# Optimization experiments

Hardware: AMD Instinct MI355X
Metric: run time of the kernel (lower is better)

## Reference

```python
import jax, jax.numpy as jnp
import numpy as np

B, L, V = 128, 32, 10000
IC, WD, H = 2048, 512, 512  # image_code_dim, word_dim, hidden_size (num_layers=1)
D = WD + IC  # GRU input dim


def setup_inputs() -> dict:
    key = jax.random.key(0)
    ks = jax.random.split(key, 10)
    image_code = jax.random.normal(ks[0], (B, IC), dtype=jnp.float32)
    captions = jax.random.randint(ks[1], (B, L), 0, V)
    cap_lens = jax.random.randint(ks[2], (B,), 2, L + 1)
    cap_lens = cap_lens.at[0].set(L)  # pin max length -> static T = L-1
    # parameters (embed/fc match init_weights uniform(-0.1,0.1); GRU/init_state ~ small random)
    embed_w = jax.random.uniform(ks[3], (V, WD), minval=-0.1, maxval=0.1, dtype=jnp.float32)
    W_ih = jax.random.normal(ks[4], (3 * H, D), dtype=jnp.float32) * 0.02
    W_hh = jax.random.normal(ks[5], (3 * H, H), dtype=jnp.float32) * 0.02
    b_ih = jnp.zeros((3 * H,), dtype=jnp.float32)
    b_hh = jnp.zeros((3 * H,), dtype=jnp.float32)
    fc_w = jax.random.uniform(ks[6], (V, H), minval=-0.1, maxval=0.1, dtype=jnp.float32)
    fc_b = jnp.zeros((V,), dtype=jnp.float32)
    init_w = jax.random.normal(ks[7], (H, IC), dtype=jnp.float32) * 0.02  # num_layers*H x IC
    init_b = jnp.zeros((H,), dtype=jnp.float32)
    return {"image_code": image_code, "captions": captions, "cap_lens": cap_lens,
            "embed_w": embed_w, "W_ih": W_ih, "W_hh": W_hh, "b_ih": b_ih, "b_hh": b_hh,
            "fc_w": fc_w, "fc_b": fc_b, "init_w": init_w, "init_b": init_b}


def _gru_decode(image_code, captions_s, lengths, h0, embed_w, W_ih, W_hh, b_ih, b_hh, fc_w, fc_b):
    T = L - 1
    emb = embed_w[captions_s]                      # (B, L, WD)
    xs = jnp.concatenate([
        jnp.broadcast_to(image_code[None], (T, B, IC)),
        jnp.transpose(emb[:, :T, :], (1, 0, 2)),   # (T, B, WD)
    ], axis=-1)                                    # (T, B, D)

    def step(h, x_t):
        gi = x_t @ W_ih.T + b_ih                   # (B, 3H)
        gh = h @ W_hh.T + b_hh                     # (B, 3H)
        i_r, i_z, i_n = jnp.split(gi, 3, axis=-1)
        h_r, h_z, h_n = jnp.split(gh, 3, axis=-1)
        r = jax.nn.sigmoid(i_r + h_r)
        z = jax.nn.sigmoid(i_z + h_z)
        n = jnp.tanh(i_n + r * h_n)
        h_new = (1.0 - z) * n + z * h
        return h_new, h_new

    _, outs = jax.lax.scan(step, h0, xs)           # (T, B, H)
    preds = jnp.einsum('tbh,vh->tbv', outs, fc_w) + fc_b  # dropout is identity in eval
    mask = jnp.arange(T)[:, None] < lengths[None, :]      # (T, B): only active steps
    preds = jnp.where(mask[:, :, None], preds, 0.0)
    return jnp.transpose(preds, (1, 0, 2))         # (B, T, V)


def reference(image_code, captions, cap_lens, embed_w, W_ih, W_hh, b_ih, b_hh, fc_w, fc_b, init_w, init_b):
    order = jnp.argsort(-cap_lens)                 # descending sort like torch.sort(..., True)
    sorted_lens = cap_lens[order]
    captions_s = captions[order]
    image_code_s = image_code[order]
    h0 = image_code_s @ init_w.T + init_b          # (B, H) (num_layers = 1)
    lengths = sorted_lens - 1
    predictions = _gru_decode(image_code_s, captions_s, lengths, h0,
                              embed_w, W_ih, W_hh, b_ih, b_hh, fc_w, fc_b)
    return predictions, captions_s, lengths, order
```

## Files before the change

### kernel.cpp

```cpp
#include <hip/hip_runtime.h>
#include <math.h>

#define B_   128
#define L_   32
#define T_   31
#define V_   10000
#define IC_  2048
#define WD_  512
#define H_   512
#define D_   2560
#define G3_  1536
#define NPAD_ 10112
#define NPROD_ 64
#define NCONS_ 158
#define NTEAM_ 2
#define SU_PFX0 1
#define SU_FCW0 17
#define SU_WHH0 (SU_FCW0 + 2528)
#define SU_N    (SU_WHH0 + 384)

typedef short short8 __attribute__((ext_vector_type(8)));
typedef float f32x4  __attribute__((ext_vector_type(4)));
typedef unsigned short ushort_t;
typedef unsigned long long ull_t;

__device__ __forceinline__ unsigned short f2bf(float f) {
    unsigned int u = __builtin_bit_cast(unsigned int, f);
    unsigned int r = (u + 0x7FFFu + ((u >> 16) & 1u)) >> 16;
    return (unsigned short)r;
}
__device__ __forceinline__ float bf2f(unsigned short h) {
    unsigned int u = ((unsigned int)h) << 16;
    return __builtin_bit_cast(float, u);
}
__device__ __forceinline__ f32x4 mfma16(short8 a, short8 b, f32x4 c) {
    return __builtin_amdgcn_mfma_f32_16x16x32_bf16(a, b, c, 0, 0, 0);
}

#define WS_ORDER  0
#define WS_LEN    512
#define WS_TOK    1024
#define WS_BAR    16896
#define WS_GIIMG  16960
#define WS_WHH    803392
#define WS_GIFULL 2376256
#define WS_OUTS   14565952
#define WS_FCW    18760256

template<bool F32>
__device__ __forceinline__ uint4 load_cvt(const void* src, size_t off) {
    if constexpr (!F32) {
        return *(const uint4*)((const unsigned short*)src + off);
    } else {
        const float* p = (const float*)src + off;
        const float4 x = *(const float4*)p;
        const float4 y = *(const float4*)(p + 4);
        union { unsigned short u[8]; uint4 v; } r;
        r.u[0]=f2bf(x.x); r.u[1]=f2bf(x.y); r.u[2]=f2bf(x.z); r.u[3]=f2bf(x.w);
        r.u[4]=f2bf(y.x); r.u[5]=f2bf(y.y); r.u[6]=f2bf(y.z); r.u[7]=f2bf(y.w);
        return r.v;
    }
}

__global__ __launch_bounds__(256) void k_setup(
    const int* __restrict__ captions,
    const int* __restrict__ cap_lens,
    const float* __restrict__ fc_w,
    const float* __restrict__ W_hh,
    const float* __restrict__ image_code,
    const float* __restrict__ W_ih,
    const float* __restrict__ b_ih,
    const float* __restrict__ init_w,
    const float* __restrict__ init_b,
    ushort_t* __restrict__ fcw_bf,
    ushort_t* __restrict__ whh_bf,
    float* __restrict__ gi_img,
    ushort_t* __restrict__ outs,
    int* __restrict__ order,
    int* __restrict__ len_i,
    int* __restrict__ tok,
    int* __restrict__ bar,
    float* __restrict__ out_tail)
{
    __shared__ __align__(16) ushort_t As[128 * 32];
    __shared__ __align__(16) ushort_t Bs[128 * 32];
    __shared__ int s_len[B_];
    __shared__ int s_ord[B_];
    const int bid = blockIdx.x;
    const int tid = threadIdx.x;

    if (bid >= SU_FCW0 && bid < SU_WHH0) {
        const int idx = (bid - SU_FCW0) * 256 + tid;
        const int row = idx >> 6;
        const int ch  = idx & 63;
        union { unsigned short u[8]; uint4 v; } r;
        if (row < V_) {
            const float* p = fc_w + (size_t)row * 512 + ch * 8;
            const float4 x = *(const float4*)p;
            const float4 y = *(const float4*)(p + 4);
            r.u[0]=f2bf(x.x); r.u[1]=f2bf(x.y); r.u[2]=f2bf(x.z); r.u[3]=f2bf(x.w);
            r.u[4]=f2bf(y.x); r.u[5]=f2bf(y.y); r.u[6]=f2bf(y.z); r.u[7]=f2bf(y.w);
        } else {
            r.v = make_uint4(0, 0, 0, 0);
        }
        *(uint4*)&fcw_bf[(size_t)row * 512 + ch * 8] = r.v;
        return;
    }
    if (bid >= SU_WHH0) {
        const int idx = (bid - SU_WHH0) * 256 + tid;
        const size_t o = (size_t)idx * 8;
        const int g = (int)(o / (48 * 512));
        const int rem = (int)(o % (48 * 512));
        const int j = rem >> 9;
        const int k = rem & 511;
        const int srow = (j >> 4) * 512 + g * 16 + (j & 15);
        const float* p = W_hh + (size_t)srow * 512 + k;
        const float4 x = *(const float4*)p;
        const float4 y = *(const float4*)(p + 4);
        union { unsigned short u[8]; uint4 v; } r;
        r.u[0]=f2bf(x.x); r.u[1]=f2bf(x.y); r.u[2]=f2bf(x.z); r.u[3]=f2bf(x.w);
        r.u[4]=f2bf(y.x); r.u[5]=f2bf(y.y); r.u[6]=f2bf(y.z); r.u[7]=f2bf(y.w);
        *(uint4*)&whh_bf[o] = r.v;
        return;
    }

    if (tid < B_) s_len[tid] = cap_lens[tid];
    __syncthreads();
    if (tid < B_) {
        const int myl = s_len[tid];
        int rank = 0;
        for (int k = 0; k < B_; ++k) {
            const int lk = s_len[k];
            if (lk > myl || (lk == myl && k < tid)) rank++;
        }
        s_ord[rank] = tid;
    }
    __syncthreads();

    if (bid == 0) {
        if (tid == 0) *bar = 0;
        if (tid < B_) {
            const int o = s_ord[tid];
            order[tid] = o;
            const int ln = s_len[o] - 1;
            len_i[tid] = ln;
            out_tail[B_ * L_ + tid]      = (float)ln;
            out_tail[B_ * L_ + B_ + tid] = (float)o;
        }
        __syncthreads();
        for (int i = tid; i < B_ * L_; i += 256) {
            const int b = i / L_, l = i % L_;
            const int c = captions[s_ord[b] * L_ + l];
            out_tail[i] = (float)c;
            if (l < T_) tok[l * B_ + b] = c;
        }
        return;
    }

    const int px = bid - SU_PFX0;
    const bool isH0 = px >= 12;
    const float* Bm = isH0 ? init_w : W_ih;
    const int ldb = isH0 ? IC_ : D_;
    const int n0 = isH0 ? (px - 12) * 128 : px * 128;
    const float* bias = isH0 ? init_b : b_ih;

    const int w = tid >> 6, lane = tid & 63, quad = lane >> 4, lr = lane & 15;
    const int srow = tid >> 2, ch = tid & 3;
    const int wm = (w & 1) * 64, wn = (w >> 1) * 64;

    const int ar0 = s_ord[srow];
    const int ar1 = s_ord[srow + 64];
    const int br0 = n0 + srow, br1 = n0 + srow + 64;

    f32x4 acc[4][4];
    const f32x4 z4 = {0.f, 0.f, 0.f, 0.f};
#pragma unroll
    for (int i = 0; i < 4; ++i)
#pragma unroll
        for (int j = 0; j < 4; ++j) acc[i][j] = z4;

    uint4 a0 = load_cvt<true>(image_code, (size_t)ar0 * IC_ + ch * 8);
    uint4 a1 = load_cvt<true>(image_code, (size_t)ar1 * IC_ + ch * 8);
    uint4 b0 = load_cvt<true>(Bm, (size_t)br0 * ldb + ch * 8);
    uint4 b1 = load_cvt<true>(Bm, (size_t)br1 * ldb + ch * 8);

    for (int k0 = 0; k0 < IC_; k0 += 32) {
        __syncthreads();
        *(uint4*)&As[(srow)      * 32 + ch * 8] = a0;
        *(uint4*)&As[(srow + 64) * 32 + ch * 8] = a1;
        *(uint4*)&Bs[(srow)      * 32 + ch * 8] = b0;
        *(uint4*)&Bs[(srow + 64) * 32 + ch * 8] = b1;
        __syncthreads();
        short8 af[4], bfr[4];
#pragma unroll
        for (int i = 0; i < 4; ++i) af[i]  = *(const short8*)&As[(wm + i * 16 + lr) * 32 + quad * 8];
#pragma unroll
        for (int j = 0; j < 4; ++j) bfr[j] = *(const short8*)&Bs[(wn + j * 16 + lr) * 32 + quad * 8];
        if (k0 + 32 < IC_) {
            a0 = load_cvt<true>(image_code, (size_t)ar0 * IC_ + k0 + 32 + ch * 8);
            a1 = load_cvt<true>(image_code, (size_t)ar1 * IC_ + k0 + 32 + ch * 8);
            b0 = load_cvt<true>(Bm, (size_t)br0 * ldb + k0 + 32 + ch * 8);
            b1 = load_cvt<true>(Bm, (size_t)br1 * ldb + k0 + 32 + ch * 8);
        }
#pragma unroll
        for (int i = 0; i < 4; ++i)
#pragma unroll
            for (int j = 0; j < 4; ++j) acc[i][j] = mfma16(af[i], bfr[j], acc[i][j]);
    }

#pragma unroll
    for (int i = 0; i < 4; ++i)
#pragma unroll
        for (int r = 0; r < 4; ++r) {
            const int m = wm + i * 16 + quad * 4 + r;
#pragma unroll
            for (int j = 0; j < 4; ++j) {
                const int n = n0 + wn + j * 16 + lr;
                const float v = acc[i][j][r] + bias[n];
                if (isH0) outs[(size_t)m * H_ + n] = f2bf(v);
                else      gi_img[(size_t)m * G3_ + n] = v;
            }
        }
}

struct EpiAdd2D {
    ushort_t* C; int ldc; const float* add; int addld; const float* bhh;
    __device__ void operator()(int m, int n, float v) const {
        const float extra = (n < 1024) ? bhh[n] : 0.f;
        C[(size_t)m * ldc + n] = f2bf(v + add[(size_t)(m & 127) * addld + n] + extra);
    }
};

template<bool AF32, bool BF32, class Epi>
__global__ __launch_bounds__(256) void gemm128(
    const void* __restrict__ A, int lda, const int* __restrict__ gidx,
    const void* __restrict__ Bm, int ldb, int K, Epi epi)
{
    __shared__ ushort_t As[128 * 32];
    __shared__ ushort_t Bs[128 * 32];
    const int tid = threadIdx.x;
    const int m0 = blockIdx.y * 128, n0 = blockIdx.x * 128;
    const int w = tid >> 6, lane = tid & 63, quad = lane >> 4, lr = lane & 15;
    const int srow = tid >> 2, ch = tid & 3;
    const int wm = (w & 1) * 64, wn = (w >> 1) * 64;

    const int ar0 = gidx ? gidx[m0 + srow]      : (m0 + srow);
    const int ar1 = gidx ? gidx[m0 + srow + 64] : (m0 + srow + 64);
    const int br0 = n0 + srow, br1 = n0 + srow + 64;

    f32x4 acc[4][4];
    const f32x4 z4 = {0.f, 0.f, 0.f, 0.f};
#pragma unroll
    for (int i = 0; i < 4; ++i)
#pragma unroll
        for (int j = 0; j < 4; ++j) acc[i][j] = z4;

    uint4 a0 = load_cvt<AF32>(A, (size_t)ar0 * lda + ch * 8);
    uint4 a1 = load_cvt<AF32>(A, (size_t)ar1 * lda + ch * 8);
    uint4 b0 = load_cvt<BF32>(Bm, (size_t)br0 * ldb + ch * 8);
    uint4 b1 = load_cvt<BF32>(Bm, (size_t)br1 * ldb + ch * 8);

    for (int k0 = 0; k0 < K; k0 += 32) {
        __syncthreads();
        *(uint4*)&As[(srow)      * 32 + ch * 8] = a0;
        *(uint4*)&As[(srow + 64) * 32 + ch * 8] = a1;
        *(uint4*)&Bs[(srow)      * 32 + ch * 8] = b0;
        *(uint4*)&Bs[(srow + 64) * 32 + ch * 8] = b1;
        __syncthreads();
        short8 af[4], bfr[4];
#pragma unroll
        for (int i = 0; i < 4; ++i) af[i]  = *(const short8*)&As[(wm + i * 16 + lr) * 32 + quad * 8];
#pragma unroll
        for (int j = 0; j < 4; ++j) bfr[j] = *(const short8*)&Bs[(wn + j * 16 + lr) * 32 + quad * 8];
        if (k0 + 32 < K) {
            a0 = load_cvt<AF32>(A, (size_t)ar0 * lda + k0 + 32 + ch * 8);
            a1 = load_cvt<AF32>(A, (size_t)ar1 * lda + k0 + 32 + ch * 8);
            b0 = load_cvt<BF32>(Bm, (size_t)br0 * ldb + k0 + 32 + ch * 8);
            b1 = load_cvt<BF32>(Bm, (size_t)br1 * ldb + k0 + 32 + ch * 8);
        }
#pragma unroll
        for (int i = 0; i < 4; ++i)
#pragma unroll
            for (int j = 0; j < 4; ++j) acc[i][j] = mfma16(af[i], bfr[j], acc[i][j]);
    }

#pragma unroll
    for (int i = 0; i < 4; ++i)
#pragma unroll
        for (int r = 0; r < 4; ++r) {
            const int m = m0 + wm + i * 16 + quad * 4 + r;
#pragma unroll
            for (int j = 0; j < 4; ++j) {
                const int n = n0 + wn + j * 16 + lr;
                epi(m, n, acc[i][j][r]);
            }
        }
}

#define PBS_STR 520
__global__ __launch_bounds__(256, 1) void k_fused(
    const ushort_t* __restrict__ whh_bf,
    const ushort_t* __restrict__ gi_full,
    const float* __restrict__ b_hh,
    ushort_t* __restrict__ outs,
    const ushort_t* __restrict__ fcw_bf,
    const float* __restrict__ fc_b,
    const int* __restrict__ len_i,
    float* __restrict__ out,
    int* __restrict__ sync)
{
    __shared__ __align__(16) ushort_t sm[43008];
    const int bid = blockIdx.x;
    const int tid = threadIdx.x;
    const int w = tid >> 6, lane = tid & 63, quad = lane >> 4, lr = lane & 15;

    if (bid < NPROD_) {
        __builtin_amdgcn_s_setprio(1);
        const int g = bid & 31;
        const int ih = bid >> 5;
        const bool leader = (bid == (ih << 5));
        ushort_t* Bs = sm;

        const ushort_t* wsrc = whh_bf + (size_t)g * 48 * 512;
        for (int i = tid; i < 48 * 64; i += 256) {
            const int row = i >> 6, c = i & 63;
            *(uint4*)&Bs[row * PBS_STR + c * 8] = *(const uint4*)&wsrc[row * 512 + c * 8];
        }
        const int cg = g * 16 + lr;
        const float bhn = b_hh[1024 + cg];
        __syncthreads();

        float hold_reg[4];
        {
            const ushort_t* h0p = outs + (size_t)ih * 64 * 512;
#pragma unroll
            for (int r = 0; r < 4; ++r)
                hold_reg[r] = bf2f(h0p[(size_t)(w * 16 + quad * 4 + r) * 512 + cg]);
        }
        ushort_t gi0[4], gi1[4], gi2[4];
#pragma unroll
        for (int r = 0; r < 4; ++r) {
            const int b = ih * 64 + w * 16 + quad * 4 + r;
            const ushort_t* p = gi_full + (size_t)b * G3_ + cg;
            gi0[r] = p[0]; gi1[r] = p[512]; gi2[r] = p[1024];
        }

        for (int step = 0; step < T_; ++step) {
            const ushort_t* hsrc = outs + (size_t)step * (128 * 512) + (size_t)ih * 64 * 512;

            uint4 hv[16];
            const ushort_t* hrow = hsrc + (size_t)(w * 16 + lr) * 512 + quad * 8;
#pragma unroll
            for (int kk = 0; kk < 16; ++kk)
                hv[kk] = *(const uint4*)(hrow + kk * 32);

            f32x4 acc[3];
#pragma unroll
            for (int j = 0; j < 3; ++j) acc[j] = (f32x4){0.f, 0.f, 0.f, 0.f};
#pragma unroll
            for (int kk = 0; kk < 16; ++kk) {
                union { uint4 v; short8 s; } cc; cc.v = hv[kk];
                const short8 af = cc.s;
#pragma unroll
                for (int j = 0; j < 3; ++j) {
                    const short8 bf = *(const short8*)&Bs[(j * 16 + lr) * PBS_STR + kk * 32 + quad * 8];
                    acc[j] = mfma16(af, bf, acc[j]);
                }
            }

            ushort_t* hdst = outs + (size_t)(step + 1) * (128 * 512);
#pragma unroll
            for (int r = 0; r < 4; ++r) {
                const int b = ih * 64 + w * 16 + quad * 4 + r;
                const float ir  = bf2f(gi0[r]);
                const float iz  = bf2f(gi1[r]);
                const float in_ = bf2f(gi2[r]);
                const float hr = acc[0][r];
                const float hz = acc[1][r];
                const float hn = acc[2][r] + bhn;
                const float rg = 1.f / (1.f + __expf(-(ir + hr)));
                const float zg = 1.f / (1.f + __expf(-(iz + hz)));
                const float nn = tanhf(in_ + rg * hn);
                const float hnew = (1.f - zg) * nn + zg * hold_reg[r];
                const unsigned int hb = (unsigned int)f2bf(hnew);
                hold_reg[r] = bf2f((unsigned short)hb);
                const unsigned int pv = (unsigned int)__shfl_xor((int)hb, 1);
                if ((lr & 1) == 0) {
                    const unsigned int word = hb | (pv << 16);
                    __hip_atomic_store((unsigned int*)&hdst[(size_t)b * 512 + cg], word,
                                       __ATOMIC_RELAXED, __HIP_MEMORY_SCOPE_AGENT);
                }
            }

            asm volatile("s_waitcnt vmcnt(0)" ::: "memory");
            __syncthreads();
            const int tgt = step + 1;
            if (tid == 0)
                __hip_atomic_store(&sync[bid * 8], tgt,
                                   __ATOMIC_RELAXED, __HIP_MEMORY_SCOPE_AGENT);

            ushort_t ng0[4], ng1[4], ng2[4];
            if (step + 1 < T_) {
                const size_t gb = (size_t)(step + 1) * 128 * G3_;
#pragma unroll
                for (int r = 0; r < 4; ++r) {
                    const int b = ih * 64 + w * 16 + quad * 4 + r;
                    const ushort_t* p = gi_full + gb + (size_t)b * G3_ + cg;
                    ng0[r] = p[0]; ng1[r] = p[512]; ng2[r] = p[1024];
                }
            }
            asm volatile("" ::: "memory");

            if (w == 0 && (step < T_ - 1 || leader)) {
                const int* pf = &sync[(ih * 32 + (lane & 31)) * 8];
                for (;;) {
                    const int v = __hip_atomic_load(pf, __ATOMIC_RELAXED, __HIP_MEMORY_SCOPE_AGENT);
                    if (__all(v >= tgt)) break;
                    __builtin_amdgcn_s_sleep(1);
                }
                if (leader && lane == 0) {
#pragma unroll
                    for (int k = 0; k < 8; ++k)
                        __hip_atomic_store(&sync[768 + k * 16 + ih], tgt,
                                           __ATOMIC_RELAXED, __HIP_MEMORY_SCOPE_AGENT);
                }
            }
            __syncthreads();
            asm volatile("" ::: "memory");

            if (step + 1 < T_) {
#pragma unroll
                for (int r = 0; r < 4; ++r) { gi0[r] = ng0[r]; gi1[r] = ng1[r]; gi2[r] = ng2[r]; }
            }
        }
    } else {
        const int cid = bid - NPROD_;
        const int nb = cid % 79;
        const int team = cid / 79;
        const int n0 = nb * 128;
        ushort_t* As = sm;
        ushort_t* Bs = sm + 4096;
        const int srow = tid >> 2, ch = tid & 3;
        const int wm = (w & 1) * 64, wn = (w >> 1) * 64;
        const ull_t* hready = (const ull_t*)&sync[768 + (cid & 7) * 16];

        float fcb[4];
#pragma unroll
        for (int j = 0; j < 4; ++j) {
            const int n = n0 + wn + j * 16 + lr;
            fcb[j] = (n < V_) ? fc_b[n] : 0.f;
        }

        for (int t = team; t < T_; t += NTEAM_) {
            if (tid == 0) {
                for (;;) {
                    const ull_t hv8 = __hip_atomic_load(hready, __ATOMIC_RELAXED, __HIP_MEMORY_SCOPE_AGENT);
                    const int l0 = (int)(unsigned int)(hv8 & 0xffffffffull);
                    const int l1 = (int)(unsigned int)(hv8 >> 32);
                    if (l0 > t && l1 > t) break;
                    __builtin_amdgcn_s_sleep(16);
                }
            }
            __syncthreads();

            const ushort_t* A = outs + (size_t)(t + 1) * (128 * 512);

            f32x4 acc[4][4];
            const f32x4 z4 = {0.f, 0.f, 0.f, 0.f};
#pragma unroll
            for (int i = 0; i < 4; ++i)
#pragma unroll
                for (int j = 0; j < 4; ++j) acc[i][j] = z4;

            uint4 a0 = *(const uint4*)&A[(size_t)srow * 512 + ch * 8];
            uint4 a1 = *(const uint4*)&A[(size_t)(srow + 64) * 512 + ch * 8];
            uint4 b0 = *(const uint4*)&fcw_bf[(size_t)(n0 + srow)      * 512 + ch * 8];
            uint4 b1 = *(const uint4*)&fcw_bf[(size_t)(n0 + srow + 64) * 512 + ch * 8];

            for (int k0 = 0; k0 < 512; k0 += 32) {
                __syncthreads();
                *(uint4*)&As[(srow)      * 32 + ch * 8] = a0;
                *(uint4*)&As[(srow + 64) * 32 + ch * 8] = a1;
                *(uint4*)&Bs[(srow)      * 32 + ch * 8] = b0;
                *(uint4*)&Bs[(srow + 64) * 32 + ch * 8] = b1;
                __syncthreads();
                short8 af[4], bfr[4];
#pragma unroll
                for (int i = 0; i < 4; ++i) af[i]  = *(const short8*)&As[(wm + i * 16 + lr) * 32 + quad * 8];
#pragma unroll
                for (int j = 0; j < 4; ++j) bfr[j] = *(const short8*)&Bs[(wn + j * 16 + lr) * 32 + quad * 8];
                if (k0 + 32 < 512) {
                    a0 = *(const uint4*)&A[(size_t)srow * 512 + k0 + 32 + ch * 8];
                    a1 = *(const uint4*)&A[(size_t)(srow + 64) * 512 + k0 + 32 + ch * 8];
                    b0 = *(const uint4*)&fcw_bf[(size_t)(n0 + srow)      * 512 + k0 + 32 + ch * 8];
                    b1 = *(const uint4*)&fcw_bf[(size_t)(n0 + srow + 64) * 512 + k0 + 32 + ch * 8];
                }
#pragma unroll
                for (int i = 0; i < 4; ++i)
#pragma unroll
                    for (int j = 0; j < 4; ++j) acc[i][j] = mfma16(af[i], bfr[j], acc[i][j]);
            }

#pragma unroll
            for (int i = 0; i < 4; ++i)
#pragma unroll
                for (int r = 0; r < 4; ++r) {
                    const int b = wm + i * 16 + quad * 4 + r;
                    const bool act = (t < len_i[b]);
                    const size_t base = (size_t)b * T_ * V_ + (size_t)t * V_;
#pragma unroll
                    for (int j = 0; j < 4; ++j) {
                        const int n = n0 + wn + j * 16 + lr;
                        if (n < V_) out[base + n] = act ? (acc[i][j][r] + fcb[j]) : 0.f;
                    }
                }
        }
    }
}

extern "C" void kernel_launch(void* const* d_in, const int* in_sizes, int n_in,
                              void* d_out, int out_size, void* d_ws, size_t ws_size,
                              hipStream_t stream) {
    const float* image_code = (const float*)d_in[0];
    const int*   captions   = (const int*)d_in[1];
    const int*   cap_lens   = (const int*)d_in[2];
    const float* embed_w    = (const float*)d_in[3];
    const float* W_ih       = (const float*)d_in[4];
    const float* W_hh       = (const float*)d_in[5];
    const float* b_ih       = (const float*)d_in[6];
    const float* b_hh       = (const float*)d_in[7];
    const float* fc_w       = (const float*)d_in[8];
    const float* fc_b       = (const float*)d_in[9];
    const float* init_w     = (const float*)d_in[10];
    const float* init_b     = (const float*)d_in[11];

    float* out = (float*)d_out;
    char* ws = (char*)d_ws;
    int*      order   = (int*)(ws + WS_ORDER);
    int*      len_i   = (int*)(ws + WS_LEN);
    int*      tok     = (int*)(ws + WS_TOK);
    int*      bar     = (int*)(ws + WS_BAR);
    float*    gi_img  = (float*)(ws + WS_GIIMG);
    ushort_t* whh_bf  = (ushort_t*)(ws + WS_WHH);
    ushort_t* gi_full = (ushort_t*)(ws + WS_GIFULL);
    ushort_t* outs_bf = (ushort_t*)(ws + WS_OUTS);
    ushort_t* fcw_bf  = (ushort_t*)(ws + WS_FCW);
    int*      sync    = (int*)(fcw_bf + ((size_t)NPAD_ - 4) * 512);

    hipLaunchKernelGGL(k_setup, dim3(SU_N), dim3(256), 0, stream,
                       captions, cap_lens, fc_w, W_hh,
                       image_code, W_ih, b_ih, init_w, init_b,
                       fcw_bf, whh_bf, gi_img, outs_bf,
                       order, len_i, tok, bar,
                       out + (size_t)B_ * T_ * V_);

    hipLaunchKernelGGL((gemm128<true, true, EpiAdd2D>), dim3(12, 31), dim3(256), 0, stream,
                       embed_w, WD_, tok, W_ih + IC_, D_, WD_,
                       EpiAdd2D{gi_full, G3_, gi_img, G3_, b_hh});

    hipLaunchKernelGGL(k_fused, dim3(NPROD_ + NCONS_), dim3(256), 0, stream,
                       whh_bf, gi_full, b_hh, outs_bf,
                       fcw_bf, fc_b, len_i, out, sync);
}
```

Before: 498.2 us.

## Fold embedding input-gate GEMM into fused persistent kernel with per-step readiness flags

Removes the separate gi GEMM launch and spreads its 372 tiles across producer and consumer blocks of the persistent fused kernel. Each finished tile bumps a per-timestep counter, and producers wait on the next step's counter before loading that step's gates, so the recurrence can start once step 0 is ready instead of after the whole GEMM. The consumer FC GEMM also moves to a K=64 padded-stride LDS tile to halve barrier count. The cost is added spin-waiting and possible stalls if later gi tiles lag behind the recurrence. The per-step gate prefetch is also dropped, so those loads now sit on the critical path.

```diff
diff --git a/kernel.cpp b/kernel.cpp
--- a/kernel.cpp
+++ b/kernel.cpp
@@ -14,6 +14,7 @@
 #define NPROD_ 64
 #define NCONS_ 158
 #define NTEAM_ 2
+#define NGITILE_ (31 * 12)
 #define SU_PFX0 1
 #define SU_FCW0 17
 #define SU_WHH0 (SU_FCW0 + 2528)
@@ -223,29 +224,23 @@
         }
 }
 
-struct EpiAdd2D {
-    ushort_t* C; int ldc; const float* add; int addld; const float* bhh;
-    __device__ void operator()(int m, int n, float v) const {
-        const float extra = (n < 1024) ? bhh[n] : 0.f;
-        C[(size_t)m * ldc + n] = f2bf(v + add[(size_t)(m & 127) * addld + n] + extra);
-    }
-};
-
-template<bool AF32, bool BF32, class Epi>
-__global__ __launch_bounds__(256) void gemm128(
-    const void* __restrict__ A, int lda, const int* __restrict__ gidx,
-    const void* __restrict__ Bm, int ldb, int K, Epi epi)
+__device__ __forceinline__ void gi_tile_worker(
+    int tile, ushort_t* sm,
+    const float* __restrict__ embed_w, const int* __restrict__ tok,
+    const float* __restrict__ W_ih_tail, const float* __restrict__ gi_img,
+    const float* __restrict__ b_hh, ushort_t* __restrict__ gi_full,
+    int* __restrict__ gidone, int tid)
 {
-    __shared__ ushort_t As[128 * 32];
-    __shared__ ushort_t Bs[128 * 32];
-    const int tid = threadIdx.x;
-    const int m0 = blockIdx.y * 128, n0 = blockIdx.x * 128;
+    const int t = tile / 12, nt = tile - t * 12;
+    const int m0 = t * 128, n0 = nt * 128;
+    ushort_t* As = sm;
+    ushort_t* Bs = sm + 4096;
     const int w = tid >> 6, lane = tid & 63, quad = lane >> 4, lr = lane & 15;
     const int srow = tid >> 2, ch = tid & 3;
     const int wm = (w & 1) * 64, wn = (w >> 1) * 64;
 
-    const int ar0 = gidx ? gidx[m0 + srow]      : (m0 + srow);
-    const int ar1 = gidx ? gidx[m0 + srow + 64] : (m0 + srow + 64);
+    const int ar0 = tok[m0 + srow];
+    const int ar1 = tok[m0 + srow + 64];
     const int br0 = n0 + srow, br1 = n0 + srow + 64;
 
     f32x4 acc[4][4];
@@ -255,12 +250,12 @@
 #pragma unroll
         for (int j = 0; j < 4; ++j) acc[i][j] = z4;
 
-    uint4 a0 = load_cvt<AF32>(A, (size_t)ar0 * lda + ch * 8);
-    uint4 a1 = load_cvt<AF32>(A, (size_t)ar1 * lda + ch * 8);
-    uint4 b0 = load_cvt<BF32>(Bm, (size_t)br0 * ldb + ch * 8);
-    uint4 b1 = load_cvt<BF32>(Bm, (size_t)br1 * ldb + ch * 8);
-
-    for (int k0 = 0; k0 < K; k0 += 32) {
+    uint4 a0 = load_cvt<true>(embed_w, (size_t)ar0 * WD_ + ch * 8);
+    uint4 a1 = load_cvt<true>(embed_w, (size_t)ar1 * WD_ + ch * 8);
+    uint4 b0 = load_cvt<true>(W_ih_tail, (size_t)br0 * D_ + ch * 8);
+    uint4 b1 = load_cvt<true>(W_ih_tail, (size_t)br1 * D_ + ch * 8);
+
+    for (int k0 = 0; k0 < WD_; k0 += 32) {
         __syncthreads();
         *(uint4*)&As[(srow)      * 32 + ch * 8] = a0;
         *(uint4*)&As[(srow + 64) * 32 + ch * 8] = a1;
@@ -272,11 +267,11 @@
         for (int i = 0; i < 4; ++i) af[i]  = *(const short8*)&As[(wm + i * 16 + lr) * 32 + quad * 8];
 #pragma unroll
         for (int j = 0; j < 4; ++j) bfr[j] = *(const short8*)&Bs[(wn + j * 16 + lr) * 32 + quad * 8];
-        if (k0 + 32 < K) {
-            a0 = load_cvt<AF32>(A, (size_t)ar0 * lda + k0 + 32 + ch * 8);
-            a1 = load_cvt<AF32>(A, (size_t)ar1 * lda + k0 + 32 + ch * 8);
-            b0 = load_cvt<BF32>(Bm, (size_t)br0 * ldb + k0 + 32 + ch * 8);
-            b1 = load_cvt<BF32>(Bm, (size_t)br1 * ldb + k0 + 32 + ch * 8);
+        if (k0 + 32 < WD_) {
+            a0 = load_cvt<true>(embed_w, (size_t)ar0 * WD_ + k0 + 32 + ch * 8);
+            a1 = load_cvt<true>(embed_w, (size_t)ar1 * WD_ + k0 + 32 + ch * 8);
+            b0 = load_cvt<true>(W_ih_tail, (size_t)br0 * D_ + k0 + 32 + ch * 8);
+            b1 = load_cvt<true>(W_ih_tail, (size_t)br1 * D_ + k0 + 32 + ch * 8);
         }
 #pragma unroll
         for (int i = 0; i < 4; ++i)
@@ -292,35 +287,57 @@
 #pragma unroll
             for (int j = 0; j < 4; ++j) {
                 const int n = n0 + wn + j * 16 + lr;
-                epi(m, n, acc[i][j][r]);
-            }
-        }
+                const float extra = (n < 1024) ? b_hh[n] : 0.f;
+                const float v = acc[i][j][r] + gi_img[(size_t)(m & 127) * G3_ + n] + extra;
+                const unsigned int hb = (unsigned int)f2bf(v);
+                const unsigned int pv = (unsigned int)__shfl_xor((int)hb, 1);
+                if ((lr & 1) == 0) {
+                    const unsigned int word = hb | (pv << 16);
+                    __hip_atomic_store((unsigned int*)&gi_full[(size_t)m * G3_ + n], word,
+                                       __ATOMIC_RELAXED, __HIP_MEMORY_SCOPE_AGENT);
+                }
+            }
+        }
+    asm volatile("s_waitcnt vmcnt(0)" ::: "memory");
+    __syncthreads();
+    if (tid == 0)
+        __hip_atomic_fetch_add(&gidone[t], 1, __ATOMIC_RELAXED, __HIP_MEMORY_SCOPE_AGENT);
 }
 
 #define PBS_STR 520
+#define CAS_STR 72
 __global__ __launch_bounds__(256, 1) void k_fused(
     const ushort_t* __restrict__ whh_bf,
-    const ushort_t* __restrict__ gi_full,
+    ushort_t* __restrict__ gi_full,
     const float* __restrict__ b_hh,
     ushort_t* __restrict__ outs,
     const ushort_t* __restrict__ fcw_bf,
     const float* __restrict__ fc_b,
     const int* __restrict__ len_i,
     float* __restrict__ out,
-    int* __restrict__ sync)
+    int* __restrict__ sync,
+    const float* __restrict__ embed_w,
+    const int* __restrict__ tok,
+    const float* __restrict__ W_ih_tail,
+    const float* __restrict__ gi_img)
 {
     __shared__ __align__(16) ushort_t sm[43008];
     const int bid = blockIdx.x;
     const int tid = threadIdx.x;
     const int w = tid >> 6, lane = tid & 63, quad = lane >> 4, lr = lane & 15;
+    int* gidone = &sync[896];
 
     if (bid < NPROD_) {
+        gi_tile_worker(bid, sm, embed_w, tok, W_ih_tail, gi_img, b_hh,
+                       gi_full, gidone, tid);
+
         __builtin_amdgcn_s_setprio(1);
         const int g = bid & 31;
         const int ih = bid >> 5;
         const bool leader = (bid == (ih << 5));
         ushort_t* Bs = sm;
 
+        __syncthreads();
         const ushort_t* wsrc = whh_bf + (size_t)g * 48 * 512;
         for (int i = tid; i < 48 * 64; i += 256) {
             const int row = i >> 6, c = i & 63;
@@ -330,6 +347,12 @@
         const float bhn = b_hh[1024 + cg];
         __syncthreads();
 
+        if (tid == 0) {
+            while (__hip_atomic_load(&gidone[0], __ATOMIC_RELAXED, __HIP_MEMORY_SCOPE_AGENT) < 12)
+                __builtin_amdgcn_s_sleep(4);
+        }
+        __syncthreads();
+
         float hold_reg[4];
         {
             const ushort_t* h0p = outs + (size_t)ih * 64 * 512;
@@ -337,16 +360,20 @@
             for (int r = 0; r < 4; ++r)
                 hold_reg[r] = bf2f(h0p[(size_t)(w * 16 + quad * 4 + r) * 512 + cg]);
         }
-        ushort_t gi0[4], gi1[4], gi2[4];
-#pragma unroll
-        for (int r = 0; r < 4; ++r) {
-            const int b = ih * 64 + w * 16 + quad * 4 + r;
-            const ushort_t* p = gi_full + (size_t)b * G3_ + cg;
-            gi0[r] = p[0]; gi1[r] = p[512]; gi2[r] = p[1024];
-        }
 
         for (int step = 0; step < T_; ++step) {
             const ushort_t* hsrc = outs + (size_t)step * (128 * 512) + (size_t)ih * 64 * 512;
+
+            ushort_t gi0[4], gi1[4], gi2[4];
+            {
+                const size_t gb = (size_t)step * 128 * G3_;
+#pragma unroll
+                for (int r = 0; r < 4; ++r) {
+                    const int b = ih * 64 + w * 16 + quad * 4 + r;
+                    const ushort_t* p = gi_full + gb + (size_t)b * G3_ + cg;
+                    gi0[r] = p[0]; gi1[r] = p[512]; gi2[r] = p[1024];
+                }
+            }
 
             uint4 hv[16];
             const ushort_t* hrow = hsrc + (size_t)(w * 16 + lr) * 512 + quad * 8;
@@ -399,23 +426,15 @@
                 __hip_atomic_store(&sync[bid * 8], tgt,
                                    __ATOMIC_RELAXED, __HIP_MEMORY_SCOPE_AGENT);
 
-            ushort_t ng0[4], ng1[4], ng2[4];
-            if (step + 1 < T_) {
-                const size_t gb = (size_t)(step + 1) * 128 * G3_;
-#pragma unroll
-                for (int r = 0; r < 4; ++r) {
-                    const int b = ih * 64 + w * 16 + quad * 4 + r;
-                    const ushort_t* p = gi_full + gb + (size_t)b * G3_ + cg;
-                    ng0[r] = p[0]; ng1[r] = p[512]; ng2[r] = p[1024];
-                }
-            }
-            asm volatile("" ::: "memory");
-
             if (w == 0 && (step < T_ - 1 || leader)) {
                 const int* pf = &sync[(ih * 32 + (lane & 31)) * 8];
+                const bool needgi = (step + 1 < T_);
                 for (;;) {
                     const int v = __hip_atomic_load(pf, __ATOMIC_RELAXED, __HIP_MEMORY_SCOPE_AGENT);
-                    if (__all(v >= tgt)) break;
+                    const int gd = (needgi && lane == 0)
+                        ? __hip_atomic_load(&gidone[step + 1], __ATOMIC_RELAXED, __HIP_MEMORY_SCOPE_AGENT)
+                        : 12;
+                    if (__all(v >= tgt) && __all(gd >= 12)) break;
                     __builtin_amdgcn_s_sleep(1);
                 }
                 if (leader && lane == 0) {
@@ -427,20 +446,21 @@
             }
             __syncthreads();
             asm volatile("" ::: "memory");
-
-            if (step + 1 < T_) {
-#pragma unroll
-                for (int r = 0; r < 4; ++r) { gi0[r] = ng0[r]; gi1[r] = ng1[r]; gi2[r] = ng2[r]; }
-            }
         }
     } else {
         const int cid = bid - NPROD_;
+
+        for (int tix = NPROD_ + cid; tix < NGITILE_; tix += NCONS_)
+            gi_tile_worker(tix, sm, embed_w, tok, W_ih_tail, gi_img, b_hh,
+                           gi_full, gidone, tid);
+        __syncthreads();
+
         const int nb = cid % 79;
         const int team = cid / 79;
         const int n0 = nb * 128;
         ushort_t* As = sm;
-        ushort_t* Bs = sm + 4096;
-        const int srow = tid >> 2, ch = tid & 3;
+        ushort_t* Bs = sm + 128 * CAS_STR;
+        const int srow = tid >> 3, ch8 = (tid & 7) * 8;
         const int wm = (w & 1) * 64, wn = (w >> 1) * 64;
         const ull_t* hready = (const ull_t*)&sync[768 + (cid & 7) * 16];
 
@@ -472,33 +492,42 @@
 #pragma unroll
                 for (int j = 0; j < 4; ++j) acc[i][j] = z4;
 
-            uint4 a0 = *(const uint4*)&A[(size_t)srow * 512 + ch * 8];
-            uint4 a1 = *(const uint4*)&A[(size_t)(srow + 64) * 512 + ch * 8];
-            uint4 b0 = *(const uint4*)&fcw_bf[(size_t)(n0 + srow)      * 512 + ch * 8];
-            uint4 b1 = *(const uint4*)&fcw_bf[(size_t)(n0 + srow + 64) * 512 + ch * 8];
-
-            for (int k0 = 0; k0 < 512; k0 += 32) {
+            uint4 av[4], bv[4];
+#pragma unroll
+            for (int p = 0; p < 4; ++p) {
+                av[p] = *(const uint4*)&A[(size_t)(srow + 32 * p) * 512 + ch8];
+                bv[p] = *(const uint4*)&fcw_bf[(size_t)(n0 + srow + 32 * p) * 512 + ch8];
+            }
+
+            for (int k0 = 0; k0 < 512; k0 += 64) {
                 __syncthreads();
-                *(uint4*)&As[(srow)      * 32 + ch * 8] = a0;
-                *(uint4*)&As[(srow + 64) * 32 + ch * 8] = a1;
-                *(uint4*)&Bs[(srow)      * 32 + ch * 8] = b0;
-                *(uint4*)&Bs[(srow + 64) * 32 + ch * 8] = b1;
+#pragma unroll
+                for (int p = 0; p < 4; ++p) {
+                    *(uint4*)&As[(srow + 32 * p) * CAS_STR + ch8] = av[p];
+                    *(uint4*)&Bs[(srow + 32 * p) * CAS_STR + ch8] = bv[p];
+                }
                 __syncthreads();
-                short8 af[4], bfr[4];
-#pragma unroll
-                for (int i = 0; i < 4; ++i) af[i]  = *(const short8*)&As[(wm + i * 16 + lr) * 32 + quad * 8];
-#pragma unroll
-                for (int j = 0; j < 4; ++j) bfr[j] = *(const short8*)&Bs[(wn + j * 16 + lr) * 32 + quad * 8];
-                if (k0 + 32 < 512) {
-                    a0 = *(const uint4*)&A[(size_t)srow * 512 + k0 + 32 + ch * 8];
-                    a1 = *(const uint4*)&A[(size_t)(srow + 64) * 512 + k0 + 32 + ch * 8];
-                    b0 = *(const uint4*)&fcw_bf[(size_t)(n0 + srow)      * 512 + k0 + 32 + ch * 8];
-                    b1 = *(const uint4*)&fcw_bf[(size_t)(n0 + srow + 64) * 512 + k0 + 32 + ch * 8];
-                }
-#pragma unroll
-                for (int i = 0; i < 4; ++i)
-#pragma unroll
-                    for (int j = 0; j < 4; ++j) acc[i][j] = mfma16(af[i], bfr[j], acc[i][j]);
+                if (k0 + 64 < 512) {
+#pragma unroll
+                    for (int p = 0; p < 4; ++p) {
+                        av[p] = *(const uint4*)&A[(size_t)(srow + 32 * p) * 512 + k0 + 64 + ch8];
+                        bv[p] = *(const uint4*)&fcw_bf[(size_t)(n0 + srow + 32 * p) * 512 + k0 + 64 + ch8];
+                    }
+                }
+#pragma unroll
+                for (int kk = 0; kk < 2; ++kk) {
+                    short8 af[4], bfr[4];
+#pragma unroll
+                    for (int i = 0; i < 4; ++i)
+                        af[i]  = *(const short8*)&As[(wm + i * 16 + lr) * CAS_STR + kk * 32 + quad * 8];
+#pragma unroll
+                    for (int j = 0; j < 4; ++j)
+                        bfr[j] = *(const short8*)&Bs[(wn + j * 16 + lr) * CAS_STR + kk * 32 + quad * 8];
+#pragma unroll
+                    for (int i = 0; i < 4; ++i)
+#pragma unroll
+                        for (int j = 0; j < 4; ++j) acc[i][j] = mfma16(af[i], bfr[j], acc[i][j]);
+                }
             }
 
 #pragma unroll
@@ -554,11 +583,8 @@
                        order, len_i, tok, bar,
                        out + (size_t)B_ * T_ * V_);
 
-    hipLaunchKernelGGL((gemm128<true, true, EpiAdd2D>), dim3(12, 31), dim3(256), 0, stream,
-                       embed_w, WD_, tok, W_ih + IC_, D_, WD_,
-                       EpiAdd2D{gi_full, G3_, gi_img, G3_, b_hh});
-
     hipLaunchKernelGGL(k_fused, dim3(NPROD_ + NCONS_), dim3(256), 0, stream,
                        whh_bf, gi_full, b_hh, outs_bf,
-                       fcw_bf, fc_b, len_i, out, sync);
-}
+                       fcw_bf, fc_b, len_i, out, sync,
+                       embed_w, tok, W_ih + IC_, gi_img);
+}
```

New measurement: 620.1 us. 24.5% more time.

## Fold embedding input-gate GEMM into setup kernel and add image gates in GRU step

Applied to the files above, without the earlier changes.

Removes the separate gemm128 launch that computed the per-timestep word-embedding input gates. Those 372 tiles now run as extra blocks inside k_setup, reading tokens straight from captions through the sort order. The image-gate term and the r/z recurrent biases are no longer folded in ahead of time; the producer adds them in fp32 registers at each step. This saves one kernel launch and the dependency between launches. In exchange, the fused kernel does a few more adds per step and loads gi_img once at its start.

```diff
diff --git a/kernel.cpp b/kernel.cpp
--- a/kernel.cpp
+++ b/kernel.cpp
@@ -15,9 +15,10 @@
 #define NCONS_ 158
 #define NTEAM_ 2
 #define SU_PFX0 1
-#define SU_FCW0 17
-#define SU_WHH0 (SU_FCW0 + 2528)
-#define SU_N    (SU_WHH0 + 384)
+#define SU_GI0  17
+#define SU_FCW0 389
+#define SU_WHH0 2917
+#define SU_N    3301
 
 typedef short short8 __attribute__((ext_vector_type(8)));
 typedef float f32x4  __attribute__((ext_vector_type(4)));
@@ -43,7 +44,7 @@
 #define WS_BAR    16896
 #define WS_GIIMG  16960
 #define WS_WHH    803392
-#define WS_GIFULL 2376256
+#define WS_GIWEMB 2376256
 #define WS_OUTS   14565952
 #define WS_FCW    18760256
 
@@ -72,13 +73,14 @@
     const float* __restrict__ b_ih,
     const float* __restrict__ init_w,
     const float* __restrict__ init_b,
+    const float* __restrict__ embed_w,
     ushort_t* __restrict__ fcw_bf,
     ushort_t* __restrict__ whh_bf,
     float* __restrict__ gi_img,
+    ushort_t* __restrict__ gi_wemb,
     ushort_t* __restrict__ outs,
     int* __restrict__ order,
     int* __restrict__ len_i,
-    int* __restrict__ tok,
     int* __restrict__ bar,
     float* __restrict__ out_tail)
 {
@@ -150,10 +152,71 @@
         __syncthreads();
         for (int i = tid; i < B_ * L_; i += 256) {
             const int b = i / L_, l = i % L_;
-            const int c = captions[s_ord[b] * L_ + l];
-            out_tail[i] = (float)c;
-            if (l < T_) tok[l * B_ + b] = c;
-        }
+            out_tail[i] = (float)captions[s_ord[b] * L_ + l];
+        }
+        return;
+    }
+
+    const int w = tid >> 6, lane = tid & 63, quad = lane >> 4, lr = lane & 15;
+    const int srow = tid >> 2, ch = tid & 3;
+    const int wm = (w & 1) * 64, wn = (w >> 1) * 64;
+
+    f32x4 acc[4][4];
+    const f32x4 z4 = {0.f, 0.f, 0.f, 0.f};
+#pragma unroll
+    for (int i = 0; i < 4; ++i)
+#pragma unroll
+        for (int j = 0; j < 4; ++j) acc[i][j] = z4;
+
+    if (bid >= SU_GI0) {
+        const int ti = bid - SU_GI0;
+        const int t = ti / 12, nt = ti - t * 12;
+        const int n0 = nt * 128;
+        const int ar0 = captions[s_ord[srow]      * L_ + t];
+        const int ar1 = captions[s_ord[srow + 64] * L_ + t];
+        const int br0 = n0 + srow, br1 = n0 + srow + 64;
+        const float* Wt = W_ih + IC_;
+
+        uint4 a0 = load_cvt<true>(embed_w, (size_t)ar0 * WD_ + ch * 8);
+        uint4 a1 = load_cvt<true>(embed_w, (size_t)ar1 * WD_ + ch * 8);
+        uint4 b0 = load_cvt<true>(Wt, (size_t)br0 * D_ + ch * 8);
+        uint4 b1 = load_cvt<true>(Wt, (size_t)br1 * D_ + ch * 8);
+
+        for (int k0 = 0; k0 < WD_; k0 += 32) {
+            __syncthreads();
+            *(uint4*)&As[(srow)      * 32 + ch * 8] = a0;
+            *(uint4*)&As[(srow + 64) * 32 + ch * 8] = a1;
+            *(uint4*)&Bs[(srow)      * 32 + ch * 8] = b0;
+            *(uint4*)&Bs[(srow + 64) * 32 + ch * 8] = b1;
+            __syncthreads();
+            short8 af[4], bfr[4];
+#pragma unroll
+            for (int i = 0; i < 4; ++i) af[i]  = *(const short8*)&As[(wm + i * 16 + lr) * 32 + quad * 8];
+#pragma unroll
+            for (int j = 0; j < 4; ++j) bfr[j] = *(const short8*)&Bs[(wn + j * 16 + lr) * 32 + quad * 8];
+            if (k0 + 32 < WD_) {
+                a0 = load_cvt<true>(embed_w, (size_t)ar0 * WD_ + k0 + 32 + ch * 8);
+                a1 = load_cvt<true>(embed_w, (size_t)ar1 * WD_ + k0 + 32 + ch * 8);
+                b0 = load_cvt<true>(Wt, (size_t)br0 * D_ + k0 + 32 + ch * 8);
+                b1 = load_cvt<true>(Wt, (size_t)br1 * D_ + k0 + 32 + ch * 8);
+            }
+#pragma unroll
+            for (int i = 0; i < 4; ++i)
+#pragma unroll
+                for (int j = 0; j < 4; ++j) acc[i][j] = mfma16(af[i], bfr[j], acc[i][j]);
+        }
+
+#pragma unroll
+        for (int i = 0; i < 4; ++i)
+#pragma unroll
+            for (int r = 0; r < 4; ++r) {
+                const int m = t * 128 + wm + i * 16 + quad * 4 + r;
+#pragma unroll
+                for (int j = 0; j < 4; ++j) {
+                    const int n = n0 + wn + j * 16 + lr;
+                    gi_wemb[(size_t)m * G3_ + n] = f2bf(acc[i][j][r]);
+                }
+            }
         return;
     }
 
@@ -164,20 +227,9 @@
     const int n0 = isH0 ? (px - 12) * 128 : px * 128;
     const float* bias = isH0 ? init_b : b_ih;
 
-    const int w = tid >> 6, lane = tid & 63, quad = lane >> 4, lr = lane & 15;
-    const int srow = tid >> 2, ch = tid & 3;
-    const int wm = (w & 1) * 64, wn = (w >> 1) * 64;
-
     const int ar0 = s_ord[srow];
     const int ar1 = s_ord[srow + 64];
     const int br0 = n0 + srow, br1 = n0 + srow + 64;
-
-    f32x4 acc[4][4];
-    const f32x4 z4 = {0.f, 0.f, 0.f, 0.f};
-#pragma unroll
-    for (int i = 0; i < 4; ++i)
-#pragma unroll
-        for (int j = 0; j < 4; ++j) acc[i][j] = z4;
 
     uint4 a0 = load_cvt<true>(image_code, (size_t)ar0 * IC_ + ch * 8);
     uint4 a1 = load_cvt<true>(image_code, (size_t)ar1 * IC_ + ch * 8);
@@ -223,91 +275,18 @@
         }
 }
 
-struct EpiAdd2D {
-    ushort_t* C; int ldc; const float* add; int addld; const float* bhh;
-    __device__ void operator()(int m, int n, float v) const {
-        const float extra = (n < 1024) ? bhh[n] : 0.f;
-        C[(size_t)m * ldc + n] = f2bf(v + add[(size_t)(m & 127) * addld + n] + extra);
-    }
-};
-
-template<bool AF32, bool BF32, class Epi>
-__global__ __launch_bounds__(256) void gemm128(
-    const void* __restrict__ A, int lda, const int* __restrict__ gidx,
-    const void* __restrict__ Bm, int ldb, int K, Epi epi)
-{
-    __shared__ ushort_t As[128 * 32];
-    __shared__ ushort_t Bs[128 * 32];
-    const int tid = threadIdx.x;
-    const int m0 = blockIdx.y * 128, n0 = blockIdx.x * 128;
-    const int w = tid >> 6, lane = tid & 63, quad = lane >> 4, lr = lane & 15;
-    const int srow = tid >> 2, ch = tid & 3;
-    const int wm = (w & 1) * 64, wn = (w >> 1) * 64;
-
-    const int ar0 = gidx ? gidx[m0 + srow]      : (m0 + srow);
-    const int ar1 = gidx ? gidx[m0 + srow + 64] : (m0 + srow + 64);
-    const int br0 = n0 + srow, br1 = n0 + srow + 64;
-
-    f32x4 acc[4][4];
-    const f32x4 z4 = {0.f, 0.f, 0.f, 0.f};
-#pragma unroll
-    for (int i = 0; i < 4; ++i)
-#pragma unroll
-        for (int j = 0; j < 4; ++j) acc[i][j] = z4;
-
-    uint4 a0 = load_cvt<AF32>(A, (size_t)ar0 * lda + ch * 8);
-    uint4 a1 = load_cvt<AF32>(A, (size_t)ar1 * lda + ch * 8);
-    uint4 b0 = load_cvt<BF32>(Bm, (size_t)br0 * ldb + ch * 8);
-    uint4 b1 = load_cvt<BF32>(Bm, (size_t)br1 * ldb + ch * 8);
-
-    for (int k0 = 0; k0 < K; k0 += 32) {
-        __syncthreads();
-        *(uint4*)&As[(srow)      * 32 + ch * 8] = a0;
-        *(uint4*)&As[(srow + 64) * 32 + ch * 8] = a1;
-        *(uint4*)&Bs[(srow)      * 32 + ch * 8] = b0;
-        *(uint4*)&Bs[(srow + 64) * 32 + ch * 8] = b1;
-        __syncthreads();
-        short8 af[4], bfr[4];
-#pragma unroll
-        for (int i = 0; i < 4; ++i) af[i]  = *(const short8*)&As[(wm + i * 16 + lr) * 32 + quad * 8];
-#pragma unroll
-        for (int j = 0; j < 4; ++j) bfr[j] = *(const short8*)&Bs[(wn + j * 16 + lr) * 32 + quad * 8];
-        if (k0 + 32 < K) {
-            a0 = load_cvt<AF32>(A, (size_t)ar0 * lda + k0 + 32 + ch * 8);
-            a1 = load_cvt<AF32>(A, (size_t)ar1 * lda + k0 + 32 + ch * 8);
-            b0 = load_cvt<BF32>(Bm, (size_t)br0 * ldb + k0 + 32 + ch * 8);
-            b1 = load_cvt<BF32>(Bm, (size_t)br1 * ldb + k0 + 32 + ch * 8);
-        }
-#pragma unroll
-        for (int i = 0; i < 4; ++i)
-#pragma unroll
-            for (int j = 0; j < 4; ++j) acc[i][j] = mfma16(af[i], bfr[j], acc[i][j]);
-    }
-
-#pragma unroll
-    for (int i = 0; i < 4; ++i)
-#pragma unroll
-        for (int r = 0; r < 4; ++r) {
-            const int m = m0 + wm + i * 16 + quad * 4 + r;
-#pragma unroll
-            for (int j = 0; j < 4; ++j) {
-                const int n = n0 + wn + j * 16 + lr;
-                epi(m, n, acc[i][j][r]);
-            }
-        }
-}
-
 #define PBS_STR 520
 __global__ __launch_bounds__(256, 1) void k_fused(
     const ushort_t* __restrict__ whh_bf,
-    const ushort_t* __restrict__ gi_full,
+    const ushort_t* __restrict__ gi_wemb,
     const float* __restrict__ b_hh,
     ushort_t* __restrict__ outs,
     const ushort_t* __restrict__ fcw_bf,
     const float* __restrict__ fc_b,
     const int* __restrict__ len_i,
     float* __restrict__ out,
-    int* __restrict__ sync)
+    int* __restrict__ sync,
+    const float* __restrict__ gi_img)
 {
     __shared__ __align__(16) ushort_t sm[43008];
     const int bid = blockIdx.x;
@@ -327,21 +306,28 @@
             *(uint4*)&Bs[row * PBS_STR + c * 8] = *(const uint4*)&wsrc[row * 512 + c * 8];
         }
         const int cg = g * 16 + lr;
+        const float bhr = b_hh[cg];
+        const float bhz = b_hh[512 + cg];
         const float bhn = b_hh[1024 + cg];
         __syncthreads();
 
+        float gim0[4], gim1[4], gim2[4];
         float hold_reg[4];
         {
             const ushort_t* h0p = outs + (size_t)ih * 64 * 512;
 #pragma unroll
-            for (int r = 0; r < 4; ++r)
+            for (int r = 0; r < 4; ++r) {
+                const int b = ih * 64 + w * 16 + quad * 4 + r;
+                const float* pim = gi_img + (size_t)b * G3_ + cg;
+                gim0[r] = pim[0]; gim1[r] = pim[512]; gim2[r] = pim[1024];
                 hold_reg[r] = bf2f(h0p[(size_t)(w * 16 + quad * 4 + r) * 512 + cg]);
+            }
         }
         ushort_t gi0[4], gi1[4], gi2[4];
 #pragma unroll
         for (int r = 0; r < 4; ++r) {
             const int b = ih * 64 + w * 16 + quad * 4 + r;
-            const ushort_t* p = gi_full + (size_t)b * G3_ + cg;
+            const ushort_t* p = gi_wemb + (size_t)b * G3_ + cg;
             gi0[r] = p[0]; gi1[r] = p[512]; gi2[r] = p[1024];
         }
 
@@ -372,9 +358,9 @@
 #pragma unroll
             for (int r = 0; r < 4; ++r) {
                 const int b = ih * 64 + w * 16 + quad * 4 + r;
-                const float ir  = bf2f(gi0[r]);
-                const float iz  = bf2f(gi1[r]);
-                const float in_ = bf2f(gi2[r]);
+                const float ir  = bf2f(gi0[r]) + gim0[r] + bhr;
+                const float iz  = bf2f(gi1[r]) + gim1[r] + bhz;
+                const float in_ = bf2f(gi2[r]) + gim2[r];
                 const float hr = acc[0][r];
                 const float hz = acc[1][r];
                 const float hn = acc[2][r] + bhn;
@@ -405,7 +391,7 @@
 #pragma unroll
                 for (int r = 0; r < 4; ++r) {
                     const int b = ih * 64 + w * 16 + quad * 4 + r;
-                    const ushort_t* p = gi_full + gb + (size_t)b * G3_ + cg;
+                    const ushort_t* p = gi_wemb + gb + (size_t)b * G3_ + cg;
                     ng0[r] = p[0]; ng1[r] = p[512]; ng2[r] = p[1024];
                 }
             }
@@ -538,27 +524,22 @@
     char* ws = (char*)d_ws;
     int*      order   = (int*)(ws + WS_ORDER);
     int*      len_i   = (int*)(ws + WS_LEN);
-    int*      tok     = (int*)(ws + WS_TOK);
     int*      bar     = (int*)(ws + WS_BAR);
     float*    gi_img  = (float*)(ws + WS_GIIMG);
     ushort_t* whh_bf  = (ushort_t*)(ws + WS_WHH);
-    ushort_t* gi_full = (ushort_t*)(ws + WS_GIFULL);
+    ushort_t* gi_wemb = (ushort_t*)(ws + WS_GIWEMB);
     ushort_t* outs_bf = (ushort_t*)(ws + WS_OUTS);
     ushort_t* fcw_bf  = (ushort_t*)(ws + WS_FCW);
     int*      sync    = (int*)(fcw_bf + ((size_t)NPAD_ - 4) * 512);
 
     hipLaunchKernelGGL(k_setup, dim3(SU_N), dim3(256), 0, stream,
                        captions, cap_lens, fc_w, W_hh,
-                       image_code, W_ih, b_ih, init_w, init_b,
-                       fcw_bf, whh_bf, gi_img, outs_bf,
-                       order, len_i, tok, bar,
+                       image_code, W_ih, b_ih, init_w, init_b, embed_w,
+                       fcw_bf, whh_bf, gi_img, gi_wemb, outs_bf,
+                       order, len_i, bar,
                        out + (size_t)B_ * T_ * V_);
 
-    hipLaunchKernelGGL((gemm128<true, true, EpiAdd2D>), dim3(12, 31), dim3(256), 0, stream,
-                       embed_w, WD_, tok, W_ih + IC_, D_, WD_,
-                       EpiAdd2D{gi_full, G3_, gi_img, G3_, b_hh});
-
     hipLaunchKernelGGL(k_fused, dim3(NPROD_ + NCONS_), dim3(256), 0, stream,
-                       whh_bf, gi_full, b_hh, outs_bf,
-                       fcw_bf, fc_b, len_i, out, sync);
-}
+                       whh_bf, gi_wemb, b_hh, outs_bf,
+                       fcw_bf, fc_b, len_i, out, sync, gi_img);
+}
```

New measurement: 463.4 us. 7.0% less time.
